# Optimization experiments

Measured on AMD Instinct MI355X. Metric: run time of the kernel, lower is better.

Reference implementation:

```python
import jax, jax.numpy as jnp
import numpy as np

B, T, D, H, L, V = 2, 1024, 1024, 16, 4, 32000
HS = D // H  # head_size = 64


def setup_inputs() -> dict:
    key = jax.random.key(0)
    ks = jax.random.split(key, 15)
    s = 0.02
    return {
        "idx": jax.random.randint(ks[0], (B, T), 0, V, dtype=jnp.int32),
        "tok_emb": jax.random.normal(ks[1], (V, D), jnp.float32) * s,
        "pos_emb": jax.random.normal(ks[2], (T, D), jnp.float32) * s,
        "Wq": jax.random.normal(ks[3], (L, H, D, HS), jnp.float32) * s,
        "Wk": jax.random.normal(ks[4], (L, H, D, HS), jnp.float32) * s,
        "Wv": jax.random.normal(ks[5], (L, H, D, HS), jnp.float32) * s,
        "Wproj": jax.random.normal(ks[6], (L, D, D), jnp.float32) * s,
        "bproj": jnp.zeros((L, D), jnp.float32),
        "W1": jax.random.normal(ks[7], (L, D, 4 * D), jnp.float32) * s,
        "b1": jnp.zeros((L, 4 * D), jnp.float32),
        "W2": jax.random.normal(ks[8], (L, 4 * D, D), jnp.float32) * s,
        "b2": jnp.zeros((L, D), jnp.float32),
        "Wlm": jax.random.normal(ks[9], (D, V), jnp.float32) * s,
        "blm": jnp.zeros((V,), jnp.float32),
    }


def reference(idx, tok_emb, pos_emb, Wq, Wk, Wv, Wproj, bproj, W1, b1, W2, b2, Wlm, blm):
    Bn, Tn = idx.shape
    Dn = tok_emb.shape[1]
    x = tok_emb[idx] + pos_emb[jnp.arange(Tn)][None, :, :]  # (B,T,D)
    causal = jnp.tril(jnp.ones((Tn, Tn), dtype=bool))
    # NOTE: original scales by C**-0.5 where C = embedding_dim (not head_size)
    scale = Dn ** -0.5
    n_layers = Wq.shape[0]
    for l in range(n_layers):
        q = jnp.einsum('btd,hdk->bhtk', x, Wq[l])
        k = jnp.einsum('btd,hdk->bhtk', x, Wk[l])
        v = jnp.einsum('btd,hdk->bhtk', x, Wv[l])
        scores = jnp.einsum('bhtk,bhsk->bhts', q, k) * scale
        scores = jnp.where(causal[None, None, :, :], scores, -jnp.inf)
        probs = jax.nn.softmax(scores, axis=-1)
        attn = jnp.einsum('bhts,bhsk->bhtk', probs, v)
        # concat heads in head order -> (B,T,H*HS)
        attn = attn.transpose(0, 2, 1, 3).reshape(Bn, Tn, Dn)
        x = x + attn @ Wproj[l] + bproj[l]
        h = jax.nn.relu(x @ W1[l] + b1[l])
        x = x + h @ W2[l] + b2[l]
    return x @ Wlm + blm  # (B,T,V) logits
```

## Files before the change

kernel.cpp:

```cpp
#include <hip/hip_runtime.h>
#include <stdint.h>

#define DEVI static __device__ __forceinline__

typedef __attribute__((ext_vector_type(8))) __bf16    bf16x8;
typedef __attribute__((ext_vector_type(8))) uint16_t  u16x8;
typedef __attribute__((ext_vector_type(4))) uint16_t  u16x4;
typedef __attribute__((ext_vector_type(4))) float     f32x4;

DEVI uint16_t f2b(float f){
  uint32_t u = __builtin_bit_cast(uint32_t, f);
  uint32_t r = u + 0x7fffu + ((u >> 16) & 1u);
  return (uint16_t)(r >> 16);
}
DEVI float b2f(uint16_t h){ return __builtin_bit_cast(float, (uint32_t)h << 16); }

DEVI void gload_lds16(const void* g, void* l){
  __builtin_amdgcn_global_load_lds((__attribute__((address_space(1))) void*)g,
                                   (__attribute__((address_space(3))) void*)l, 16, 0, 0);
}
DEVI bf16x8 frag_ld(const void* base, int byteoff){
  const u16x8* p = (const u16x8*)((const char*)base + byteoff);
  return __builtin_bit_cast(bf16x8, *p);
}

__global__ __launch_bounds__(256) void transpose_f32_bf16(
    const float* __restrict__ in, uint16_t* __restrict__ out,
    int ld_in, int ld_out,
    long long in_z, long long out_zA, long long out_zB, int zdiv)
{
  __shared__ float tile[64][65];
  const int r0 = blockIdx.x * 64, c0 = blockIdx.y * 64;
  const int z  = blockIdx.z;
  const float* inp = in + (long long)z * in_z;
  uint16_t* outp = out + (long long)(z / zdiv) * out_zA + (long long)(z % zdiv) * out_zB;
  const int tx = threadIdx.x & 63, ty = threadIdx.x >> 6;
  #pragma unroll
  for (int i = 0; i < 16; i++){
    int r = i * 4 + ty;
    tile[r][tx] = inp[(long long)(r0 + r) * ld_in + (c0 + tx)];
  }
  __syncthreads();
  const int rp = (threadIdx.x & 31) * 2;
  const int cy = threadIdx.x >> 5;
  #pragma unroll
  for (int i = 0; i < 8; i++){
    int c = i * 8 + cy;
    uint32_t v = (uint32_t)f2b(tile[rp][c]) | ((uint32_t)f2b(tile[rp + 1][c]) << 16);
    *(uint32_t*)(outp + (long long)(c0 + c) * ld_out + (r0 + rp)) = v;
  }
}

__global__ __launch_bounds__(256) void embed_kernel(
    const int* __restrict__ idx, const float* __restrict__ tok,
    const float* __restrict__ pos, float* __restrict__ xf, uint16_t* __restrict__ xb)
{
  const int t = blockIdx.x;
  const int d = threadIdx.x * 4;
  const int token = idx[t];
  const int tp = t & 1023;
  const float4 tv = *(const float4*)(tok + (size_t)token * 1024 + d);
  const float4 pv = *(const float4*)(pos + (size_t)tp * 1024 + d);
  float4 s; s.x = tv.x + pv.x; s.y = tv.y + pv.y; s.z = tv.z + pv.z; s.w = tv.w + pv.w;
  *(float4*)(xf + (size_t)t * 1024 + d) = s;
  uint16_t* o = xb + (size_t)t * 1024 + d;
  o[0] = f2b(s.x); o[1] = f2b(s.y); o[2] = f2b(s.z); o[3] = f2b(s.w);
}

__global__ __launch_bounds__(256) void split_kernel(
    const float* __restrict__ xf, const uint16_t* __restrict__ xhi, uint16_t* __restrict__ xlo)
{
  const int i = (blockIdx.x * 256 + threadIdx.x) * 4;
  #pragma unroll
  for (int j = 0; j < 4; j++) xlo[i + j] = f2b(xf[i + j] - b2f(xhi[i + j]));
}

template<bool DUAL, bool SPLITK, bool BIAS, bool RES, bool RELU, bool OUTF, bool OUTB, bool QSCALE>
__global__ __launch_bounds__(256, DUAL ? 2 : 3) void gemm_bt(
    const uint16_t* __restrict__ A, const uint16_t* __restrict__ A2,
    const uint16_t* __restrict__ Bt,
    const float* __restrict__ bias, const float* __restrict__ res,
    float* __restrict__ outf, uint16_t* __restrict__ outb,
    int M, int N, int K)
{
  __shared__ __align__(16) uint16_t As[(DUAL ? 2 : 1) * 128 * 64];
  __shared__ __align__(16) uint16_t Bs[128 * 64];
  const int tid = threadIdx.x, lane = tid & 63, wid = tid >> 6;

  const int Mt = M >> 7;
  int flat = blockIdx.x;
  int kidx = 0;
  if constexpr (SPLITK){ kidx = flat & 1; flat >>= 1; }
  const int total = SPLITK ? (gridDim.x >> 1) : gridDim.x;
  const int wg = (flat & 7) * (total >> 3) + (flat >> 3);
  const int bm = (wg % Mt) * 128, bn = (wg / Mt) * 128;
  int k0 = 0, k1 = K;
  if constexpr (SPLITK){ const int Kh = K >> 1; k0 = kidx * Kh; k1 = k0 + Kh; }
  float* outp = outf;
  if constexpr (SPLITK) outp = outf + (size_t)kidx * M * N;

  const uint16_t* gA[4]; const uint16_t* gA2[4]; const uint16_t* gB[4];
  #pragma unroll
  for (int i = 0; i < 4; i++){
    int c = i * 256 + tid;
    int row = c >> 3;
    int p = (c * 16) ^ ((row & 7) << 4);
    int off = (p >> 1) & 63;
    gA[i] = A  + (size_t)(bm + row) * K + off;
    if constexpr (DUAL) gA2[i] = A2 + (size_t)(bm + row) * K + off;
    gB[i] = Bt + (size_t)(bn + row) * K + off;
  }

  f32x4 acc[4][4];
  const f32x4 fz = {0.f, 0.f, 0.f, 0.f};
  #pragma unroll
  for (int a = 0; a < 4; a++)
    #pragma unroll
    for (int n = 0; n < 4; n++) acc[a][n] = fz;

  const int lrow = lane & 15, lk2 = (lane >> 4) * 16;
  const int wr = (wid >> 1) * 64, wc = (wid & 1) * 64;

  for (int kt = k0; kt < k1; kt += 64){
    #pragma unroll
    for (int i = 0; i < 4; i++)
      gload_lds16(gA[i] + kt, (char*)As + (i * 256 + wid * 64) * 16);
    if constexpr (DUAL){
      #pragma unroll
      for (int i = 0; i < 4; i++)
        gload_lds16(gA2[i] + kt, (char*)(As + 8192) + (i * 256 + wid * 64) * 16);
    }
    #pragma unroll
    for (int i = 0; i < 4; i++)
      gload_lds16(gB[i] + kt, (char*)Bs + (i * 256 + wid * 64) * 16);
    __syncthreads();
    #pragma unroll
    for (int kk = 0; kk < 2; kk++){
      bf16x8 af[4], bfv[4];
      #pragma unroll
      for (int mf = 0; mf < 4; mf++){
        int row = wr + mf * 16 + lrow;
        af[mf] = frag_ld(As, (row * 128 + kk * 64 + lk2) ^ ((row & 7) << 4));
      }
      #pragma unroll
      for (int nf = 0; nf < 4; nf++){
        int row = wc + nf * 16 + lrow;
        bfv[nf] = frag_ld(Bs, (row * 128 + kk * 64 + lk2) ^ ((row & 7) << 4));
      }
      #pragma unroll
      for (int mf = 0; mf < 4; mf++)
        #pragma unroll
        for (int nf = 0; nf < 4; nf++)
          acc[mf][nf] = __builtin_amdgcn_mfma_f32_16x16x32_bf16(af[mf], bfv[nf], acc[mf][nf], 0, 0, 0);
      if constexpr (DUAL){
        bf16x8 af2[4];
        #pragma unroll
        for (int mf = 0; mf < 4; mf++){
          int row = wr + mf * 16 + lrow;
          af2[mf] = frag_ld(As + 8192, (row * 128 + kk * 64 + lk2) ^ ((row & 7) << 4));
        }
        #pragma unroll
        for (int mf = 0; mf < 4; mf++)
          #pragma unroll
          for (int nf = 0; nf < 4; nf++)
            acc[mf][nf] = __builtin_amdgcn_mfma_f32_16x16x32_bf16(af2[mf], bfv[nf], acc[mf][nf], 0, 0, 0);
      }
    }
    __syncthreads();
  }

  #pragma unroll
  for (int mf = 0; mf < 4; mf++){
    const int row0 = bm + wr + mf * 16 + (lane >> 4) * 4;
    #pragma unroll
    for (int nf = 0; nf < 4; nf++){
      const int col = bn + wc + nf * 16 + (lane & 15);
      float bv = 0.f;
      if constexpr (BIAS) bv = bias[col];
      float qs = 1.0f;
      if constexpr (QSCALE) qs = (col < 1024) ? 0.03125f : 1.0f;
      #pragma unroll
      for (int j = 0; j < 4; j++){
        float v = acc[mf][nf][j] + bv;
        size_t oi = (size_t)(row0 + j) * N + col;
        if constexpr (RES)  v += res[oi];
        if constexpr (RELU) v = fmaxf(v, 0.f);
        if constexpr (OUTF) outp[oi] = v;
        if constexpr (OUTB) outb[oi] = f2b(v * qs);
      }
    }
  }
}

__global__ __launch_bounds__(256) void reduce_sk(
    const float* __restrict__ p, const float* __restrict__ bias,
    float* __restrict__ xf, uint16_t* __restrict__ xb, int MN, int N)
{
  const int i = (blockIdx.x * 256 + threadIdx.x) * 4;
  const float4 a = *(const float4*)(p + i);
  const float4 b = *(const float4*)(p + MN + i);
  const int col = i & (N - 1);
  const float4 bv = *(const float4*)(bias + col);
  float4 x = *(float4*)(xf + i);
  x.x += a.x + b.x + bv.x;
  x.y += a.y + b.y + bv.y;
  x.z += a.z + b.z + bv.z;
  x.w += a.w + b.w + bv.w;
  *(float4*)(xf + i) = x;
  uint16_t* o = xb + i;
  o[0] = f2b(x.x); o[1] = f2b(x.y); o[2] = f2b(x.z); o[3] = f2b(x.w);
}

__global__ __launch_bounds__(256, 2) void attn_kernel(
    const uint16_t* __restrict__ qkv, uint16_t* __restrict__ out)
{
  const int bi = blockIdx.x;
  const int b  = bi >> 8;
  const int jj = bi & 255;
  const int h  = jj >> 4;
  int q64 = jj & 15;
  if (b) q64 = 15 - q64;

  __shared__ __align__(16) uint16_t Qs[64 * 64];
  __shared__ __align__(16) uint16_t Ks[128 * 64];
  __shared__ __align__(16) uint16_t Vt[64 * 128];
  __shared__ __align__(16) uint16_t Ps[64 * 128];

  const int tid = threadIdx.x, lane = tid & 63, wid = tid >> 6;
  const size_t bt0 = (size_t)b * 1024;

  int rowC[4], offC[4];
  #pragma unroll
  for (int i = 0; i < 4; i++){
    int c = i * 256 + tid;
    int row = c >> 3;
    int p = (c * 16) ^ ((row & 7) << 4);
    rowC[i] = row; offC[i] = (p >> 1) & 63;
  }

  #pragma unroll
  for (int i = 0; i < 2; i++)
    gload_lds16(qkv + (bt0 + q64 * 64 + rowC[i]) * 3072 + h * 64 + offC[i],
                (char*)Qs + (i * 256 + wid * 64) * 16);
  __syncthreads();

  const int lrow = lane & 15, lk2 = (lane >> 4) * 16, g4 = (lane >> 4) * 4;

  bf16x8 aq[2];
  {
    int row = wid * 16 + lrow;
    #pragma unroll
    for (int kk = 0; kk < 2; kk++)
      aq[kk] = frag_ld(Qs, (row * 128 + kk * 64 + lk2) ^ ((row & 7) << 4));
  }

  float m_run[4], l_run[4];
  f32x4 acc_o[4];
  const f32x4 fz = {0.f, 0.f, 0.f, 0.f};
  #pragma unroll
  for (int j = 0; j < 4; j++){ m_run[j] = -1e30f; l_run[j] = 0.f; acc_o[j] = fz; }

  const int tpV = (tid >> 4) * 2, d0V = (tid & 15) * 4;
  const int nkt = q64 >> 1;

  for (int kt = 0; kt <= nkt; ++kt){
    __syncthreads();
    #pragma unroll
    for (int i = 0; i < 4; i++)
      gload_lds16(qkv + (bt0 + kt * 128 + rowC[i]) * 3072 + 1024 + h * 64 + offC[i],
                  (char*)Ks + (i * 256 + wid * 64) * 16);
    #pragma unroll
    for (int i = 0; i < 4; i++){
      const int t = i * 32 + tpV;
      const uint16_t* src = qkv + (bt0 + kt * 128 + t) * 3072 + 2048 + h * 64 + d0V;
      const u16x4 v0 = *(const u16x4*)src;
      const u16x4 v1 = *(const u16x4*)(src + 3072);
      #pragma unroll
      for (int dd = 0; dd < 4; dd++){
        const int d = d0V + dd;
        const int byte = (d * 256 + t * 2) ^ ((((d >> 3) ^ d) & 15) << 4);
        *(uint32_t*)((char*)Vt + byte) = (uint32_t)v0[dd] | ((uint32_t)v1[dd] << 16);
      }
    }
    __syncthreads();

    f32x4 sf[8];
    #pragma unroll
    for (int n = 0; n < 8; n++) sf[n] = fz;
    __builtin_amdgcn_s_setprio(1);
    #pragma unroll
    for (int kk = 0; kk < 2; kk++){
      #pragma unroll
      for (int nf = 0; nf < 8; nf++){
        const int row = nf * 16 + lrow;
        const bf16x8 bk = frag_ld(Ks, (row * 128 + kk * 64 + lk2) ^ ((row & 7) << 4));
        sf[nf] = __builtin_amdgcn_mfma_f32_16x16x32_bf16(aq[kk], bk, sf[nf], 0, 0, 0);
      }
    }
    __builtin_amdgcn_s_setprio(0);

    const bool diag = (kt == nkt);
    #pragma unroll
    for (int j = 0; j < 4; j++){
      float pm = -1e30f;
      if (diag){
        const int rg = q64 * 64 + wid * 16 + g4 + j;
        #pragma unroll
        for (int nf = 0; nf < 8; nf++){
          const int cg = kt * 128 + nf * 16 + lrow;
          const float v = (cg <= rg) ? sf[nf][j] : -1e30f;
          sf[nf][j] = v;
          pm = fmaxf(pm, v);
        }
      } else {
        #pragma unroll
        for (int nf = 0; nf < 8; nf++) pm = fmaxf(pm, sf[nf][j]);
      }
      #pragma unroll
      for (int mk = 1; mk < 16; mk <<= 1) pm = fmaxf(pm, __shfl_xor(pm, mk));
      const float mnew = fmaxf(m_run[j], pm);
      const float corr = __expf(m_run[j] - mnew);
      m_run[j] = mnew;
      float ps = 0.f;
      #pragma unroll
      for (int nf = 0; nf < 8; nf++){
        const float p = __expf(sf[nf][j] - mnew);
        sf[nf][j] = p;
        ps += p;
      }
      #pragma unroll
      for (int mk = 1; mk < 16; mk <<= 1) ps += __shfl_xor(ps, mk);
      l_run[j] = l_run[j] * corr + ps;
      #pragma unroll
      for (int nh = 0; nh < 4; nh++) acc_o[nh][j] *= corr;
      const int rl = wid * 16 + g4 + j;
      const int sw = (((rl >> 3) ^ rl) & 15) << 4;
      #pragma unroll
      for (int nf = 0; nf < 8; nf++){
        const int byte = (rl * 256 + (nf * 16 + lrow) * 2) ^ sw;
        *(uint16_t*)((char*)Ps + byte) = f2b(sf[nf][j]);
      }
    }
    __syncthreads();

    __builtin_amdgcn_s_setprio(1);
    #pragma unroll
    for (int kk = 0; kk < 4; kk++){
      const int row = wid * 16 + lrow;
      const bf16x8 pa = frag_ld(Ps, (row * 256 + kk * 64 + lk2) ^ ((((row >> 3) ^ row) & 15) << 4));
      #pragma unroll
      for (int nh = 0; nh < 4; nh++){
        const int n = nh * 16 + lrow;
        const bf16x8 vb = frag_ld(Vt, (n * 256 + kk * 64 + lk2) ^ ((((n >> 3) ^ n) & 15) << 4));
        acc_o[nh] = __builtin_amdgcn_mfma_f32_16x16x32_bf16(pa, vb, acc_o[nh], 0, 0, 0);
      }
    }
    __builtin_amdgcn_s_setprio(0);
  }

  #pragma unroll
  for (int j = 0; j < 4; j++){
    const float inv = 1.f / l_run[j];
    const int rg = q64 * 64 + wid * 16 + g4 + j;
    #pragma unroll
    for (int nh = 0; nh < 4; nh++)
      out[(bt0 + rg) * 1024 + h * 64 + nh * 16 + lrow] = f2b(acc_o[nh][j] * inv);
  }
}

extern "C" void kernel_launch(void* const* d_in, const int* in_sizes, int n_in,
                              void* d_out, int out_size, void* d_ws, size_t ws_size,
                              hipStream_t stream)
{
  const int*   idx   = (const int*)  d_in[0];
  const float* tok   = (const float*)d_in[1];
  const float* pos   = (const float*)d_in[2];
  const float* Wq    = (const float*)d_in[3];
  const float* Wk    = (const float*)d_in[4];
  const float* Wv    = (const float*)d_in[5];
  const float* Wproj = (const float*)d_in[6];
  const float* bproj = (const float*)d_in[7];
  const float* W1    = (const float*)d_in[8];
  const float* b1    = (const float*)d_in[9];
  const float* W2    = (const float*)d_in[10];
  const float* b2    = (const float*)d_in[11];
  const float* Wlm   = (const float*)d_in[12];
  const float* blm   = (const float*)d_in[13];
  float* out = (float*)d_out;

  char* ws = (char*)d_ws;
  size_t off = 0;
  auto alloc = [&](size_t bytes){ void* p = ws + off; off += (bytes + 255) & ~(size_t)255; return p; };
  uint16_t* qkvT   = (uint16_t*)alloc((size_t)4 * 3072 * 1024 * 2);
  uint16_t* WprojT = (uint16_t*)alloc((size_t)4 * 1024 * 1024 * 2);
  uint16_t* W1T    = (uint16_t*)alloc((size_t)4 * 4096 * 1024 * 2);
  uint16_t* W2T    = (uint16_t*)alloc((size_t)4 * 1024 * 4096 * 2);
  uint16_t* WlmT   = (uint16_t*)alloc((size_t)32000 * 1024 * 2);
  float*    xf     = (float*)   alloc((size_t)2048 * 1024 * 4);
  uint16_t* xb     = (uint16_t*)alloc((size_t)2048 * 1024 * 2);
  uint16_t* xlo    = (uint16_t*)alloc((size_t)2048 * 1024 * 2);
  uint16_t* qkv_a  = (uint16_t*)alloc((size_t)2048 * 3072 * 2);
  uint16_t* attnb  = (uint16_t*)alloc((size_t)2048 * 1024 * 2);
  uint16_t* hb     = (uint16_t*)alloc((size_t)2048 * 4096 * 2);
  float*    psum   = (float*)   alloc((size_t)2 * 2048 * 1024 * 4);
  (void)ws_size; (void)in_sizes; (void)n_in; (void)out_size;

  const dim3 tb(256);
  const int MN = 2048 * 1024;

  transpose_f32_bf16<<<dim3(16, 1, 64), tb, 0, stream>>>(Wq, qkvT,                 64, 1024,
      65536LL, 3072LL * 1024, 64LL * 1024, 16);
  transpose_f32_bf16<<<dim3(16, 1, 64), tb, 0, stream>>>(Wk, qkvT + 1024 * 1024,   64, 1024,
      65536LL, 3072LL * 1024, 64LL * 1024, 16);
  transpose_f32_bf16<<<dim3(16, 1, 64), tb, 0, stream>>>(Wv, qkvT + 2048 * 1024,   64, 1024,
      65536LL, 3072LL * 1024, 64LL * 1024, 16);
  transpose_f32_bf16<<<dim3(16, 16, 4), tb, 0, stream>>>(Wproj, WprojT, 1024, 1024,
      1048576LL, 1048576LL, 0LL, 1);
  transpose_f32_bf16<<<dim3(16, 64, 4), tb, 0, stream>>>(W1, W1T, 4096, 1024,
      4194304LL, 4194304LL, 0LL, 1);
  transpose_f32_bf16<<<dim3(64, 16, 4), tb, 0, stream>>>(W2, W2T, 1024, 4096,
      4194304LL, 4194304LL, 0LL, 1);
  transpose_f32_bf16<<<dim3(16, 500, 1), tb, 0, stream>>>(Wlm, WlmT, 32000, 1024,
      0LL, 0LL, 0LL, 1);

  embed_kernel<<<dim3(2048), tb, 0, stream>>>(idx, tok, pos, xf, xb);

  for (int l = 0; l < 4; ++l){
    const uint16_t* qkvT_l = qkvT + (size_t)l * 3072 * 1024;
    gemm_bt<false, false, false, false, false, false, true, true><<<dim3(384), tb, 0, stream>>>(
        xb, nullptr, qkvT_l, nullptr, nullptr, nullptr, qkv_a, 2048, 3072, 1024);
    attn_kernel<<<dim3(512), tb, 0, stream>>>(qkv_a, attnb);
    gemm_bt<false, true, false, false, false, true, false, false><<<dim3(256), tb, 0, stream>>>(
        attnb, nullptr, WprojT + (size_t)l * 1048576, nullptr, nullptr, psum, nullptr, 2048, 1024, 1024);
    reduce_sk<<<dim3(2048), tb, 0, stream>>>(psum, bproj + l * 1024, xf, xb, MN, 1024);
    gemm_bt<false, false, true, false, true, false, true, false><<<dim3(512), tb, 0, stream>>>(
        xb, nullptr, W1T + (size_t)l * 4194304, b1 + l * 4096, nullptr, nullptr, hb, 2048, 4096, 1024);
    gemm_bt<false, true, false, false, false, true, false, false><<<dim3(256), tb, 0, stream>>>(
        hb, nullptr, W2T + (size_t)l * 4194304, nullptr, nullptr, psum, nullptr, 2048, 1024, 4096);
    reduce_sk<<<dim3(2048), tb, 0, stream>>>(psum, b2 + l * 1024, xf, xb, MN, 1024);
  }

  split_kernel<<<dim3(2048), tb, 0, stream>>>(xf, xb, xlo);
  gemm_bt<true, false, true, false, false, true, false, false><<<dim3(4000), tb, 0, stream>>>(
      xb, xlo, WlmT, blm, nullptr, out, nullptr, 2048, 32000, 1024);
}
```

Baseline: 1.016 ms.

## Switch bf16 pipeline to fp16 and drop split-precision LM head pass

Converts all weights, activations and MFMA calls from bf16 to fp16. Because fp16 has more mantissa bits, the LM-head GEMM drops its hi/lo split of the activations, so the split kernel and one of its two MFMA passes go away. The freed LDS is used to double-buffer A/B tiles in that GEMM, overlapping loads with compute. fp16's narrower exponent range risks overflow or underflow in activations or attention scores, though values at these scales are likely safe.

Measured after the change: 952.9 us. 1.07x faster.

```diff
diff --git a/kernel.cpp b/kernel.cpp
--- a/kernel.cpp
+++ b/kernel.cpp
@@ -3,28 +3,23 @@
 
 #define DEVI static __device__ __forceinline__
 
-typedef __attribute__((ext_vector_type(8))) __bf16    bf16x8;
+typedef __attribute__((ext_vector_type(8))) _Float16  f16x8;
 typedef __attribute__((ext_vector_type(8))) uint16_t  u16x8;
 typedef __attribute__((ext_vector_type(4))) uint16_t  u16x4;
 typedef __attribute__((ext_vector_type(4))) float     f32x4;
 
-DEVI uint16_t f2b(float f){
-  uint32_t u = __builtin_bit_cast(uint32_t, f);
-  uint32_t r = u + 0x7fffu + ((u >> 16) & 1u);
-  return (uint16_t)(r >> 16);
-}
-DEVI float b2f(uint16_t h){ return __builtin_bit_cast(float, (uint32_t)h << 16); }
+DEVI uint16_t f2h(float f){ return __builtin_bit_cast(uint16_t, (_Float16)f); }
 
 DEVI void gload_lds16(const void* g, void* l){
   __builtin_amdgcn_global_load_lds((__attribute__((address_space(1))) void*)g,
                                    (__attribute__((address_space(3))) void*)l, 16, 0, 0);
 }
-DEVI bf16x8 frag_ld(const void* base, int byteoff){
+DEVI f16x8 frag_ld(const void* base, int byteoff){
   const u16x8* p = (const u16x8*)((const char*)base + byteoff);
-  return __builtin_bit_cast(bf16x8, *p);
-}
-
-__global__ __launch_bounds__(256) void transpose_f32_bf16(
+  return __builtin_bit_cast(f16x8, *p);
+}
+
+__global__ __launch_bounds__(256) void transpose_f32_f16(
     const float* __restrict__ in, uint16_t* __restrict__ out,
     int ld_in, int ld_out,
     long long in_z, long long out_zA, long long out_zB, int zdiv)
@@ -46,7 +41,7 @@
   #pragma unroll
   for (int i = 0; i < 8; i++){
     int c = i * 8 + cy;
-    uint32_t v = (uint32_t)f2b(tile[rp][c]) | ((uint32_t)f2b(tile[rp + 1][c]) << 16);
+    uint32_t v = (uint32_t)f2h(tile[rp][c]) | ((uint32_t)f2h(tile[rp + 1][c]) << 16);
     *(uint32_t*)(outp + (long long)(c0 + c) * ld_out + (r0 + rp)) = v;
   }
 }
@@ -64,27 +59,18 @@
   float4 s; s.x = tv.x + pv.x; s.y = tv.y + pv.y; s.z = tv.z + pv.z; s.w = tv.w + pv.w;
   *(float4*)(xf + (size_t)t * 1024 + d) = s;
   uint16_t* o = xb + (size_t)t * 1024 + d;
-  o[0] = f2b(s.x); o[1] = f2b(s.y); o[2] = f2b(s.z); o[3] = f2b(s.w);
-}
-
-__global__ __launch_bounds__(256) void split_kernel(
-    const float* __restrict__ xf, const uint16_t* __restrict__ xhi, uint16_t* __restrict__ xlo)
-{
-  const int i = (blockIdx.x * 256 + threadIdx.x) * 4;
-  #pragma unroll
-  for (int j = 0; j < 4; j++) xlo[i + j] = f2b(xf[i + j] - b2f(xhi[i + j]));
-}
-
-template<bool DUAL, bool SPLITK, bool BIAS, bool RES, bool RELU, bool OUTF, bool OUTB, bool QSCALE>
-__global__ __launch_bounds__(256, DUAL ? 2 : 3) void gemm_bt(
-    const uint16_t* __restrict__ A, const uint16_t* __restrict__ A2,
-    const uint16_t* __restrict__ Bt,
+  o[0] = f2h(s.x); o[1] = f2h(s.y); o[2] = f2h(s.z); o[3] = f2h(s.w);
+}
+
+template<bool DBUF, bool SPLITK, bool BIAS, bool RES, bool RELU, bool OUTF, bool OUTB, bool QSCALE>
+__global__ __launch_bounds__(256, DBUF ? 2 : 3) void gemm_bt(
+    const uint16_t* __restrict__ A, const uint16_t* __restrict__ Bt,
     const float* __restrict__ bias, const float* __restrict__ res,
     float* __restrict__ outf, uint16_t* __restrict__ outb,
     int M, int N, int K)
 {
-  __shared__ __align__(16) uint16_t As[(DUAL ? 2 : 1) * 128 * 64];
-  __shared__ __align__(16) uint16_t Bs[128 * 64];
+  __shared__ __align__(16) uint16_t As[(DBUF ? 2 : 1) * 128 * 64];
+  __shared__ __align__(16) uint16_t Bs[(DBUF ? 2 : 1) * 128 * 64];
   const int tid = threadIdx.x, lane = tid & 63, wid = tid >> 6;
 
   const int Mt = M >> 7;
@@ -99,7 +85,7 @@
   float* outp = outf;
   if constexpr (SPLITK) outp = outf + (size_t)kidx * M * N;
 
-  const uint16_t* gA[4]; const uint16_t* gA2[4]; const uint16_t* gB[4];
+  const uint16_t* gA[4]; const uint16_t* gB[4];
   #pragma unroll
   for (int i = 0; i < 4; i++){
     int c = i * 256 + tid;
@@ -107,7 +93,6 @@
     int p = (c * 16) ^ ((row & 7) << 4);
     int off = (p >> 1) & 63;
     gA[i] = A  + (size_t)(bm + row) * K + off;
-    if constexpr (DUAL) gA2[i] = A2 + (size_t)(bm + row) * K + off;
     gB[i] = Bt + (size_t)(bn + row) * K + off;
   }
 
@@ -121,52 +106,58 @@
   const int lrow = lane & 15, lk2 = (lane >> 4) * 16;
   const int wr = (wid >> 1) * 64, wc = (wid & 1) * 64;
 
-  for (int kt = k0; kt < k1; kt += 64){
+  auto stage = [&](int kt, int half){
     #pragma unroll
     for (int i = 0; i < 4; i++)
-      gload_lds16(gA[i] + kt, (char*)As + (i * 256 + wid * 64) * 16);
-    if constexpr (DUAL){
-      #pragma unroll
-      for (int i = 0; i < 4; i++)
-        gload_lds16(gA2[i] + kt, (char*)(As + 8192) + (i * 256 + wid * 64) * 16);
-    }
+      gload_lds16(gA[i] + kt, (char*)As + half * 16384 + (i * 256 + wid * 64) * 16);
     #pragma unroll
     for (int i = 0; i < 4; i++)
-      gload_lds16(gB[i] + kt, (char*)Bs + (i * 256 + wid * 64) * 16);
-    __syncthreads();
+      gload_lds16(gB[i] + kt, (char*)Bs + half * 16384 + (i * 256 + wid * 64) * 16);
+  };
+  auto compute = [&](int half){
     #pragma unroll
     for (int kk = 0; kk < 2; kk++){
-      bf16x8 af[4], bfv[4];
+      f16x8 af[4], bfv[4];
       #pragma unroll
       for (int mf = 0; mf < 4; mf++){
         int row = wr + mf * 16 + lrow;
-        af[mf] = frag_ld(As, (row * 128 + kk * 64 + lk2) ^ ((row & 7) << 4));
+        af[mf] = frag_ld((char*)As + half * 16384, (row * 128 + kk * 64 + lk2) ^ ((row & 7) << 4));
       }
       #pragma unroll
       for (int nf = 0; nf < 4; nf++){
         int row = wc + nf * 16 + lrow;
-        bfv[nf] = frag_ld(Bs, (row * 128 + kk * 64 + lk2) ^ ((row & 7) << 4));
+        bfv[nf] = frag_ld((char*)Bs + half * 16384, (row * 128 + kk * 64 + lk2) ^ ((row & 7) << 4));
       }
       #pragma unroll
       for (int mf = 0; mf < 4; mf++)
         #pragma unroll
         for (int nf = 0; nf < 4; nf++)
-          acc[mf][nf] = __builtin_amdgcn_mfma_f32_16x16x32_bf16(af[mf], bfv[nf], acc[mf][nf], 0, 0, 0);
-      if constexpr (DUAL){
-        bf16x8 af2[4];
-        #pragma unroll
-        for (int mf = 0; mf < 4; mf++){
-          int row = wr + mf * 16 + lrow;
-          af2[mf] = frag_ld(As + 8192, (row * 128 + kk * 64 + lk2) ^ ((row & 7) << 4));
-        }
-        #pragma unroll
-        for (int mf = 0; mf < 4; mf++)
-          #pragma unroll
-          for (int nf = 0; nf < 4; nf++)
-            acc[mf][nf] = __builtin_amdgcn_mfma_f32_16x16x32_bf16(af2[mf], bfv[nf], acc[mf][nf], 0, 0, 0);
-      }
-    }
+          acc[mf][nf] = __builtin_amdgcn_mfma_f32_16x16x32_f16(af[mf], bfv[nf], acc[mf][nf], 0, 0, 0);
+    }
+  };
+
+  if constexpr (DBUF){
+    stage(k0, 0);
     __syncthreads();
+    for (int kt = k0; kt < k1; kt += 128){
+      if (kt + 64 < k1) stage(kt + 64, 1);
+      compute(0);
+      __syncthreads();
+      if (kt + 128 < k1){
+        stage(kt + 128, 0);
+        compute(1);
+        __syncthreads();
+      } else if (kt + 64 < k1){
+        compute(1);
+      }
+    }
+  } else {
+    for (int kt = k0; kt < k1; kt += 64){
+      stage(kt, 0);
+      __syncthreads();
+      compute(0);
+      __syncthreads();
+    }
   }
 
   #pragma unroll
@@ -186,7 +177,7 @@
         if constexpr (RES)  v += res[oi];
         if constexpr (RELU) v = fmaxf(v, 0.f);
         if constexpr (OUTF) outp[oi] = v;
-        if constexpr (OUTB) outb[oi] = f2b(v * qs);
+        if constexpr (OUTB) outb[oi] = f2h(v * qs);
       }
     }
   }
@@ -208,7 +199,7 @@
   x.w += a.w + b.w + bv.w;
   *(float4*)(xf + i) = x;
   uint16_t* o = xb + i;
-  o[0] = f2b(x.x); o[1] = f2b(x.y); o[2] = f2b(x.z); o[3] = f2b(x.w);
+  o[0] = f2h(x.x); o[1] = f2h(x.y); o[2] = f2h(x.z); o[3] = f2h(x.w);
 }
 
 __global__ __launch_bounds__(256, 2) void attn_kernel(
@@ -246,7 +237,7 @@
 
   const int lrow = lane & 15, lk2 = (lane >> 4) * 16, g4 = (lane >> 4) * 4;
 
-  bf16x8 aq[2];
+  f16x8 aq[2];
   {
     int row = wid * 16 + lrow;
     #pragma unroll
@@ -293,8 +284,8 @@
       #pragma unroll
       for (int nf = 0; nf < 8; nf++){
         const int row = nf * 16 + lrow;
-        const bf16x8 bk = frag_ld(Ks, (row * 128 + kk * 64 + lk2) ^ ((row & 7) << 4));
-        sf[nf] = __builtin_amdgcn_mfma_f32_16x16x32_bf16(aq[kk], bk, sf[nf], 0, 0, 0);
+        const f16x8 bk = frag_ld(Ks, (row * 128 + kk * 64 + lk2) ^ ((row & 7) << 4));
+        sf[nf] = __builtin_amdgcn_mfma_f32_16x16x32_f16(aq[kk], bk, sf[nf], 0, 0, 0);
       }
     }
     __builtin_amdgcn_s_setprio(0);
@@ -338,7 +329,7 @@
       #pragma unroll
       for (int nf = 0; nf < 8; nf++){
         const int byte = (rl * 256 + (nf * 16 + lrow) * 2) ^ sw;
-        *(uint16_t*)((char*)Ps + byte) = f2b(sf[nf][j]);
+        *(uint16_t*)((char*)Ps + byte) = f2h(sf[nf][j]);
       }
     }
     __syncthreads();
@@ -347,12 +338,12 @@
     #pragma unroll
     for (int kk = 0; kk < 4; kk++){
       const int row = wid * 16 + lrow;
-      const bf16x8 pa = frag_ld(Ps, (row * 256 + kk * 64 + lk2) ^ ((((row >> 3) ^ row) & 15) << 4));
+      const f16x8 pa = frag_ld(Ps, (row * 256 + kk * 64 + lk2) ^ ((((row >> 3) ^ row) & 15) << 4));
       #pragma unroll
       for (int nh = 0; nh < 4; nh++){
         const int n = nh * 16 + lrow;
-        const bf16x8 vb = frag_ld(Vt, (n * 256 + kk * 64 + lk2) ^ ((((n >> 3) ^ n) & 15) << 4));
-        acc_o[nh] = __builtin_amdgcn_mfma_f32_16x16x32_bf16(pa, vb, acc_o[nh], 0, 0, 0);
+        const f16x8 vb = frag_ld(Vt, (n * 256 + kk * 64 + lk2) ^ ((((n >> 3) ^ n) & 15) << 4));
+        acc_o[nh] = __builtin_amdgcn_mfma_f32_16x16x32_f16(pa, vb, acc_o[nh], 0, 0, 0);
       }
     }
     __builtin_amdgcn_s_setprio(0);
@@ -364,7 +355,7 @@
     const int rg = q64 * 64 + wid * 16 + g4 + j;
     #pragma unroll
     for (int nh = 0; nh < 4; nh++)
-      out[(bt0 + rg) * 1024 + h * 64 + nh * 16 + lrow] = f2b(acc_o[nh][j] * inv);
+      out[(bt0 + rg) * 1024 + h * 64 + nh * 16 + lrow] = f2h(acc_o[nh][j] * inv);
   }
 }
 
@@ -398,7 +389,6 @@
   uint16_t* WlmT   = (uint16_t*)alloc((size_t)32000 * 1024 * 2);
   float*    xf     = (float*)   alloc((size_t)2048 * 1024 * 4);
   uint16_t* xb     = (uint16_t*)alloc((size_t)2048 * 1024 * 2);
-  uint16_t* xlo    = (uint16_t*)alloc((size_t)2048 * 1024 * 2);
   uint16_t* qkv_a  = (uint16_t*)alloc((size_t)2048 * 3072 * 2);
   uint16_t* attnb  = (uint16_t*)alloc((size_t)2048 * 1024 * 2);
   uint16_t* hb     = (uint16_t*)alloc((size_t)2048 * 4096 * 2);
@@ -408,19 +398,19 @@
   const dim3 tb(256);
   const int MN = 2048 * 1024;
 
-  transpose_f32_bf16<<<dim3(16, 1, 64), tb, 0, stream>>>(Wq, qkvT,                 64, 1024,
+  transpose_f32_f16<<<dim3(16, 1, 64), tb, 0, stream>>>(Wq, qkvT,                 64, 1024,
       65536LL, 3072LL * 1024, 64LL * 1024, 16);
-  transpose_f32_bf16<<<dim3(16, 1, 64), tb, 0, stream>>>(Wk, qkvT + 1024 * 1024,   64, 1024,
+  transpose_f32_f16<<<dim3(16, 1, 64), tb, 0, stream>>>(Wk, qkvT + 1024 * 1024,   64, 1024,
       65536LL, 3072LL * 1024, 64LL * 1024, 16);
-  transpose_f32_bf16<<<dim3(16, 1, 64), tb, 0, stream>>>(Wv, qkvT + 2048 * 1024,   64, 1024,
+  transpose_f32_f16<<<dim3(16, 1, 64), tb, 0, stream>>>(Wv, qkvT + 2048 * 1024,   64, 1024,
       65536LL, 3072LL * 1024, 64LL * 1024, 16);
-  transpose_f32_bf16<<<dim3(16, 16, 4), tb, 0, stream>>>(Wproj, WprojT, 1024, 1024,
+  transpose_f32_f16<<<dim3(16, 16, 4), tb, 0, stream>>>(Wproj, WprojT, 1024, 1024,
       1048576LL, 1048576LL, 0LL, 1);
-  transpose_f32_bf16<<<dim3(16, 64, 4), tb, 0, stream>>>(W1, W1T, 4096, 1024,
+  transpose_f32_f16<<<dim3(16, 64, 4), tb, 0, stream>>>(W1, W1T, 4096, 1024,
       4194304LL, 4194304LL, 0LL, 1);
-  transpose_f32_bf16<<<dim3(64, 16, 4), tb, 0, stream>>>(W2, W2T, 1024, 4096,
+  transpose_f32_f16<<<dim3(64, 16, 4), tb, 0, stream>>>(W2, W2T, 1024, 4096,
       4194304LL, 4194304LL, 0LL, 1);
-  transpose_f32_bf16<<<dim3(16, 500, 1), tb, 0, stream>>>(Wlm, WlmT, 32000, 1024,
+  transpose_f32_f16<<<dim3(16, 500, 1), tb, 0, stream>>>(Wlm, WlmT, 32000, 1024,
       0LL, 0LL, 0LL, 1);
 
   embed_kernel<<<dim3(2048), tb, 0, stream>>>(idx, tok, pos, xf, xb);
@@ -428,19 +418,18 @@
   for (int l = 0; l < 4; ++l){
     const uint16_t* qkvT_l = qkvT + (size_t)l * 3072 * 1024;
     gemm_bt<false, false, false, false, false, false, true, true><<<dim3(384), tb, 0, stream>>>(
-        xb, nullptr, qkvT_l, nullptr, nullptr, nullptr, qkv_a, 2048, 3072, 1024);
+        xb, qkvT_l, nullptr, nullptr, nullptr, qkv_a, 2048, 3072, 1024);
     attn_kernel<<<dim3(512), tb, 0, stream>>>(qkv_a, attnb);
     gemm_bt<false, true, false, false, false, true, false, false><<<dim3(256), tb, 0, stream>>>(
-        attnb, nullptr, WprojT + (size_t)l * 1048576, nullptr, nullptr, psum, nullptr, 2048, 1024, 1024);
+        attnb, WprojT + (size_t)l * 1048576, nullptr, nullptr, psum, nullptr, 2048, 1024, 1024);
     reduce_sk<<<dim3(2048), tb, 0, stream>>>(psum, bproj + l * 1024, xf, xb, MN, 1024);
     gemm_bt<false, false, true, false, true, false, true, false><<<dim3(512), tb, 0, stream>>>(
-        xb, nullptr, W1T + (size_t)l * 4194304, b1 + l * 4096, nullptr, nullptr, hb, 2048, 4096, 1024);
+        xb, W1T + (size_t)l * 4194304, b1 + l * 4096, nullptr, nullptr, hb, 2048, 4096, 1024);
     gemm_bt<false, true, false, false, false, true, false, false><<<dim3(256), tb, 0, stream>>>(
-        hb, nullptr, W2T + (size_t)l * 4194304, nullptr, nullptr, psum, nullptr, 2048, 1024, 4096);
+        hb, W2T + (size_t)l * 4194304, nullptr, nullptr, psum, nullptr, 2048, 1024, 4096);
     reduce_sk<<<dim3(2048), tb, 0, stream>>>(psum, b2 + l * 1024, xf, xb, MN, 1024);
   }
 
-  split_kernel<<<dim3(2048), tb, 0, stream>>>(xf, xb, xlo);
   gemm_bt<true, false, true, false, false, true, false, false><<<dim3(4000), tb, 0, stream>>>(
-      xb, xlo, WlmT, blm, nullptr, out, nullptr, 2048, 32000, 1024);
-}
+      xb, WlmT, blm, nullptr, out, nullptr, 2048, 32000, 1024);
+}
```
